# Kernel optimization log

Hardware: AMD Instinct MI355X
Metric: run time of the kernel (lower is better)

Reference implementation:

```python
import jax, jax.numpy as jnp
import numpy as np

N, D_IN, D_OUT = 100000, 256, 256
R, E, B = 8, 40000, 4
LN_EPS = 1e-5


def setup_inputs() -> dict:
    key = jax.random.key(0)
    ks = jax.random.split(key, 6)
    x = jax.random.normal(ks[0], (N, D_IN), dtype=jnp.float32)
    edge_index = jax.random.randint(ks[1], (R, 2, E), 0, N, dtype=jnp.int64)
    bases = jax.random.normal(ks[2], (B, D_IN, D_OUT), dtype=jnp.float32) * 0.01
    coefficients = jax.random.normal(ks[3], (R, B), dtype=jnp.float32) * 0.01
    bound = 1.0 / np.sqrt(D_IN)
    w_self = jax.random.uniform(ks[4], (D_IN, D_OUT), minval=-bound, maxval=bound, dtype=jnp.float32)
    b_self = jax.random.uniform(ks[5], (D_OUT,), minval=-bound, maxval=bound, dtype=jnp.float32)
    ln_gamma = jnp.ones((D_OUT,), dtype=jnp.float32)
    ln_beta = jnp.zeros((D_OUT,), dtype=jnp.float32)
    return {"x": x, "edge_index": edge_index, "bases": bases,
            "coefficients": coefficients, "w_self": w_self, "b_self": b_self,
            "ln_gamma": ln_gamma, "ln_beta": ln_beta}


def reference(x, edge_index, bases, coefficients, w_self, b_self, ln_gamma, ln_beta):
    n = x.shape[0]
    # self loop
    h = x @ w_self + b_self                                   # (N, D_OUT)
    # basis-composed per-relation weights
    W = jnp.einsum('rb,bio->rio', coefficients, bases)        # (R, D_IN, D_OUT)
    src = edge_index[:, 0]                                    # (R, E)
    dst = edge_index[:, 1]                                    # (R, E)
    msg = jnp.einsum('red,rdo->reo', x[src], W)               # (R, E, D_OUT)
    seg = jax.vmap(lambda d, m: jax.ops.segment_sum(m, d, num_segments=n))(dst, msg)
    deg = jax.vmap(lambda d: jax.ops.segment_sum(jnp.ones(d.shape, x.dtype), d, num_segments=n))(dst)
    deg = jnp.maximum(deg, 1.0)                               # clamp(min=1)
    h = h + (seg / deg[..., None]).sum(axis=0)
    # LayerNorm(SiLU(h)); dropout is identity in eval
    a = jax.nn.silu(h)
    mean = a.mean(axis=-1, keepdims=True)
    var = ((a - mean) ** 2).mean(axis=-1, keepdims=True)
    return (a - mean) * jax.lax.rsqrt(var + LN_EPS) * ln_gamma + ln_beta
```

## Files before the change

### kernel.cpp

```cpp
#include <hip/hip_runtime.h>
#include <hip/hip_bf16.h>

#define N_NODES 100000
#define D 256
#define R_REL 8
#define E_EDGES 40000
#define LN_EPS 1e-5f
#define ETOT (R_REL * E_EDGES)
#define SCAN_CH 1024
#define SCAN_NB ((N_NODES + SCAN_CH - 1) / SCAN_CH)
#define NROWT ((N_NODES + 127) / 128)
#define NWG (NROWT * 10)

typedef __attribute__((ext_vector_type(8))) short short8;
typedef __attribute__((ext_vector_type(4))) float f32x4;
typedef unsigned char uchar;

__device__ inline ushort bf16u(float f) {
    __hip_bfloat16 h = __float2bfloat16(f);
    return *reinterpret_cast<ushort*>(&h);
}
__device__ inline float bf2f(ushort u) { return __uint_as_float(((unsigned)u) << 16); }

__global__ __launch_bounds__(256) void k_prepB(const float* __restrict__ w_self,
                                               const float* __restrict__ bases,
                                               ushort* __restrict__ BT) {
    __shared__ float tile[64][65];
    int ot = blockIdx.x >> 2, dt = blockIdx.x & 3;
    int o0 = ot * 64, d0 = dt * 64;
    int m = o0 >> 8;
    const float* src = (m == 0) ? w_self : bases + (size_t)(m - 1) * D * D;
    int ol0 = o0 & 255;
    int t = threadIdx.x;
    int cl = t & 63, rw = t >> 6;
    for (int i = 0; i < 16; ++i) {
        int dl = i * 4 + rw;
        tile[dl][cl] = src[(size_t)(d0 + dl) * D + ol0 + cl];
    }
    __syncthreads();
    for (int i = 0; i < 16; ++i) {
        int ol = i * 4 + rw;
        BT[(size_t)(o0 + ol) * D + d0 + cl] = bf16u(tile[cl][ol]);
    }
}

__global__ __launch_bounds__(256) void k_prepX(const float* __restrict__ x,
                                               ushort* __restrict__ xb) {
    size_t idx = (size_t)blockIdx.x * 256 + threadIdx.x;
    const float4* xp = (const float4*)(x + idx * 8);
    float4 f0 = xp[0], f1 = xp[1];
    short8 v;
    v[0] = (short)bf16u(f0.x); v[1] = (short)bf16u(f0.y);
    v[2] = (short)bf16u(f0.z); v[3] = (short)bf16u(f0.w);
    v[4] = (short)bf16u(f1.x); v[5] = (short)bf16u(f1.y);
    v[6] = (short)bf16u(f1.z); v[7] = (short)bf16u(f1.w);
    *(short8*)(xb + idx * 8) = v;
}

__global__ void k_count(const int* __restrict__ ei, int* __restrict__ cnt) {
    int idx = blockIdx.x * blockDim.x + threadIdx.x;
    if (idx >= ETOT) return;
    int r = idx / E_EDGES, e = idx % E_EDGES;
    int dst = ei[(r * 2 + 1) * E_EDGES + e];
    atomicAdd(&cnt[dst], 1);
}

__global__ __launch_bounds__(256) void k_scanA(const int* __restrict__ cnt,
                                               int* __restrict__ start,
                                               int* __restrict__ sumsA) {
    __shared__ int sc[256];
    int t = threadIdx.x;
    int base = blockIdx.x * SCAN_CH + t * 4;
    int v0 = (base + 0 < N_NODES) ? cnt[base + 0] : 0;
    int v1 = (base + 1 < N_NODES) ? cnt[base + 1] : 0;
    int v2 = (base + 2 < N_NODES) ? cnt[base + 2] : 0;
    int v3 = (base + 3 < N_NODES) ? cnt[base + 3] : 0;
    int ts = v0 + v1 + v2 + v3;
    sc[t] = ts;
    __syncthreads();
    for (int off = 1; off < 256; off <<= 1) {
        int val = (t >= off) ? sc[t - off] : 0;
        __syncthreads();
        sc[t] += val;
        __syncthreads();
    }
    int excl = sc[t] - ts;
    if (base + 0 < N_NODES) start[base + 0] = excl;
    if (base + 1 < N_NODES) start[base + 1] = excl + v0;
    if (base + 2 < N_NODES) start[base + 2] = excl + v0 + v1;
    if (base + 3 < N_NODES) start[base + 3] = excl + v0 + v1 + v2;
    if (t == 255) sumsA[blockIdx.x] = sc[255];
}

__global__ __launch_bounds__(256) void k_scanB(const int* __restrict__ sumsA,
                                               int* __restrict__ sumsB) {
    __shared__ int sc[256];
    int t = threadIdx.x;
    int i0 = t * 4;
    int v0 = (i0 + 0 < SCAN_NB) ? sumsA[i0 + 0] : 0;
    int v1 = (i0 + 1 < SCAN_NB) ? sumsA[i0 + 1] : 0;
    int v2 = (i0 + 2 < SCAN_NB) ? sumsA[i0 + 2] : 0;
    int v3 = (i0 + 3 < SCAN_NB) ? sumsA[i0 + 3] : 0;
    int ts = v0 + v1 + v2 + v3;
    sc[t] = ts;
    __syncthreads();
    for (int off = 1; off < 256; off <<= 1) {
        int val = (t >= off) ? sc[t - off] : 0;
        __syncthreads();
        sc[t] += val;
        __syncthreads();
    }
    int excl = sc[t] - ts;
    if (i0 + 0 < SCAN_NB) sumsB[i0 + 0] = excl;
    if (i0 + 1 < SCAN_NB) sumsB[i0 + 1] = excl + v0;
    if (i0 + 2 < SCAN_NB) sumsB[i0 + 2] = excl + v0 + v1;
    if (i0 + 3 < SCAN_NB) sumsB[i0 + 3] = excl + v0 + v1 + v2;
}

__global__ __launch_bounds__(256) void k_scanC(int* __restrict__ start,
                                               const int* __restrict__ sumsB,
                                               int* __restrict__ cursor) {
    int idx = blockIdx.x * blockDim.x + threadIdx.x;
    if (idx < N_NODES) {
        int v = start[idx] + sumsB[idx / SCAN_CH];
        start[idx] = v;
        cursor[idx] = v;
    }
    if (idx == 0) start[N_NODES] = ETOT;
}

__global__ void k_scatter(const int* __restrict__ ei, int* __restrict__ cursor,
                          int* __restrict__ payload) {
    int idx = blockIdx.x * blockDim.x + threadIdx.x;
    if (idx >= ETOT) return;
    int r = idx / E_EDGES, e = idx % E_EDGES;
    int src = ei[r * 2 * E_EDGES + e];
    int dst = ei[(r * 2 + 1) * E_EDGES + e];
    int pos = atomicAdd(&cursor[dst], 1);
    payload[pos] = (r << 20) | src;
}

__global__ __launch_bounds__(256, 2) void k_gemm(const ushort* __restrict__ xb,
                                                 const ushort* __restrict__ BT,
                                                 ushort* __restrict__ hb,
                                                 uchar* __restrict__ U) {
    __shared__ ushort As[2][128 * 64];
    __shared__ ushort Bs[2][128 * 64];
    int t = threadIdx.x;

    const int q = NWG / 8, r8 = NWG % 8;
    int dd = blockIdx.x;
    int xcd = dd & 7, slot = dd >> 3;
    int wgid = (xcd < r8 ? xcd * (q + 1) : r8 * (q + 1) + (xcd - r8) * q) + slot;
    int rowtile = wgid / 10, pass = wgid % 10;
    int row0 = rowtile * 128;

    int l = t & 63, w = t >> 6;
    int wr = w >> 1, wc = w & 1;
    int lr = l & 15, lg = l >> 4;

    auto stageA = [&](int buf, int kt) {
#pragma unroll
        for (int p = 0; p < 4; ++p) {
            int o = p * 4096 + t * 16;
            int rowA = o >> 7;
            int colb = (o & 127) ^ ((rowA & 7) << 4);
            int srcrow = min(row0 + rowA, N_NODES - 1);
            const char* gp = (const char*)xb + ((size_t)srcrow * D + kt * 64) * 2 + colb;
            char* lp = (char*)&As[buf][0] + p * 4096 + (t >> 6) * 1024;
            __builtin_amdgcn_global_load_lds(
                (const __attribute__((address_space(1))) void*)gp,
                (__attribute__((address_space(3))) void*)lp, 16, 0, 0);
        }
    };
    auto stageB = [&](int buf, int kt) {
#pragma unroll
        for (int p = 0; p < 4; ++p) {
            int o = p * 4096 + t * 16;
            int rowB = o >> 7;
            int colb = (o & 127) ^ ((rowB & 7) << 4);
            const char* gp = (const char*)BT +
                ((size_t)(pass * 128 + rowB) * D + kt * 64) * 2 + colb;
            char* lp = (char*)&Bs[buf][0] + p * 4096 + (t >> 6) * 1024;
            __builtin_amdgcn_global_load_lds(
                (const __attribute__((address_space(1))) void*)gp,
                (__attribute__((address_space(3))) void*)lp, 16, 0, 0);
        }
    };

    f32x4 acc[4][4] = {};
    stageA(0, 0); stageB(0, 0);
    int buf = 0;
    for (int kt = 0; kt < 4; ++kt) {
        __syncthreads();
        if (kt < 3) { stageA(buf ^ 1, kt + 1); stageB(buf ^ 1, kt + 1); }
#pragma unroll
        for (int kk = 0; kk < 2; ++kk) {
            int kb = kk * 64 + lg * 16;
            short8 a[4], b[4];
#pragma unroll
            for (int mi = 0; mi < 4; ++mi) {
                int row = wr * 64 + mi * 16 + lr;
                a[mi] = *(const short8*)((const char*)&As[buf][0] +
                         row * 128 + (kb ^ ((row & 7) << 4)));
            }
#pragma unroll
            for (int ni = 0; ni < 4; ++ni) {
                int rb = wc * 64 + ni * 16 + lr;
                b[ni] = *(const short8*)((const char*)&Bs[buf][0] +
                         rb * 128 + (kb ^ ((rb & 7) << 4)));
            }
#pragma unroll
            for (int mi = 0; mi < 4; ++mi)
#pragma unroll
                for (int ni = 0; ni < 4; ++ni)
                    acc[mi][ni] = __builtin_amdgcn_mfma_f32_16x16x32_bf16(
                        a[mi], b[ni], acc[mi][ni], 0, 0, 0);
        }
        buf ^= 1;
    }

    if (pass < 2) {
        int colbase = pass * 128 + wc * 64 + lr;
#pragma unroll
        for (int mi = 0; mi < 4; ++mi)
#pragma unroll
            for (int j = 0; j < 4; ++j) {
                int row = row0 + wr * 64 + mi * 16 + lg * 4 + j;
                if (row < N_NODES) {
                    ushort* op = hb + (size_t)row * D + colbase;
#pragma unroll
                    for (int ni = 0; ni < 4; ++ni) op[ni * 16] = bf16u(acc[mi][ni][j]);
                }
            }
    } else {
        int pl = pass - 2;
        int plane = pl >> 1;
        int colbase = (pl & 1) * 128 + wc * 64 + lr;
#pragma unroll
        for (int mi = 0; mi < 4; ++mi)
#pragma unroll
            for (int j = 0; j < 4; ++j) {
                int row = row0 + wr * 64 + mi * 16 + lg * 4 + j;
                if (row < N_NODES) {
                    uchar* up = U + (size_t)row * 1024 + plane * 256 + colbase;
                    unsigned p01 = __builtin_amdgcn_cvt_pk_fp8_f32(
                        acc[mi][0][j] * 64.0f, acc[mi][1][j] * 64.0f, 0, 0);
                    unsigned p23 = __builtin_amdgcn_cvt_pk_fp8_f32(
                        acc[mi][2][j] * 64.0f, acc[mi][3][j] * 64.0f, 0, 0);
                    up[0]  = (uchar)(p01 & 0xFF);
                    up[16] = (uchar)((p01 >> 8) & 0xFF);
                    up[32] = (uchar)(p23 & 0xFF);
                    up[48] = (uchar)((p23 >> 8) & 0xFF);
                }
            }
    }
}

__global__ __launch_bounds__(256) void k_final(float* __restrict__ out,
                                               const ushort* __restrict__ hb,
                                               const uchar* __restrict__ U,
                                               const int* __restrict__ start,
                                               const int* __restrict__ payload,
                                               const float* __restrict__ coeff,
                                               const float* __restrict__ bias,
                                               const float* __restrict__ gamma,
                                               const float* __restrict__ beta) {
    __shared__ float cf[32];
    int t = threadIdx.x;
    if (t < 32) cf[t] = coeff[t];
    __syncthreads();
    int lane = t & 63, w = t >> 6;
    int n = blockIdx.x * 4 + w;
    int s = start[n], e = start[n + 1];

    unsigned long long cnt64 = 0;
    for (int p = s; p < e; ++p)
        cnt64 += 1ull << ((payload[p] >> 20) * 8);

    float msg[4] = {0.f, 0.f, 0.f, 0.f};
    for (int p = s; p < e; ++p) {
        int pk = payload[p];
        int r = pk >> 20, src = pk & 0xFFFFF;
        float dg = (float)((unsigned)(cnt64 >> (r * 8)) & 255u);
        float inv = __builtin_amdgcn_rcpf(dg) * 0.015625f;
        float4 wv = *(const float4*)&cf[r * 4];
        const uchar* up = U + (size_t)src * 1024 + lane * 4;
        unsigned v0 = *(const unsigned*)(up);
        unsigned v1 = *(const unsigned*)(up + 256);
        unsigned v2 = *(const unsigned*)(up + 512);
        unsigned v3 = *(const unsigned*)(up + 768);
        float w0 = wv.x * inv, w1 = wv.y * inv, w2 = wv.z * inv, w3 = wv.w * inv;
        msg[0] += w0 * __builtin_amdgcn_cvt_f32_fp8(v0, 0)
                + w1 * __builtin_amdgcn_cvt_f32_fp8(v1, 0)
                + w2 * __builtin_amdgcn_cvt_f32_fp8(v2, 0)
                + w3 * __builtin_amdgcn_cvt_f32_fp8(v3, 0);
        msg[1] += w0 * __builtin_amdgcn_cvt_f32_fp8(v0, 1)
                + w1 * __builtin_amdgcn_cvt_f32_fp8(v1, 1)
                + w2 * __builtin_amdgcn_cvt_f32_fp8(v2, 1)
                + w3 * __builtin_amdgcn_cvt_f32_fp8(v3, 1);
        msg[2] += w0 * __builtin_amdgcn_cvt_f32_fp8(v0, 2)
                + w1 * __builtin_amdgcn_cvt_f32_fp8(v1, 2)
                + w2 * __builtin_amdgcn_cvt_f32_fp8(v2, 2)
                + w3 * __builtin_amdgcn_cvt_f32_fp8(v3, 2);
        msg[3] += w0 * __builtin_amdgcn_cvt_f32_fp8(v0, 3)
                + w1 * __builtin_amdgcn_cvt_f32_fp8(v1, 3)
                + w2 * __builtin_amdgcn_cvt_f32_fp8(v2, 3)
                + w3 * __builtin_amdgcn_cvt_f32_fp8(v3, 3);
    }

    int col = lane * 4;
    size_t ro = (size_t)n * D + col;
    ushort4 hu = *(const ushort4*)&hb[ro];
    float4 bv = *(const float4*)&bias[col];
    float a[4];
    a[0] = bf2f(hu.x) + bv.x + msg[0];
    a[1] = bf2f(hu.y) + bv.y + msg[1];
    a[2] = bf2f(hu.z) + bv.z + msg[2];
    a[3] = bf2f(hu.w) + bv.w + msg[3];
    float sum = 0.f, sq = 0.f;
#pragma unroll
    for (int j = 0; j < 4; ++j) {
        a[j] = a[j] / (1.f + expf(-a[j]));
        sum += a[j]; sq += a[j] * a[j];
    }
#pragma unroll
    for (int off = 32; off >= 1; off >>= 1) {
        sum += __shfl_xor(sum, off, 64);
        sq  += __shfl_xor(sq,  off, 64);
    }
    float mean = sum * (1.0f / 256.0f);
    float var = sq * (1.0f / 256.0f) - mean * mean;
    float rs = rsqrtf(var + LN_EPS);
    float4 g4 = *(const float4*)&gamma[col];
    float4 b4 = *(const float4*)&beta[col];
    float4 o4;
    o4.x = (a[0] - mean) * rs * g4.x + b4.x;
    o4.y = (a[1] - mean) * rs * g4.y + b4.y;
    o4.z = (a[2] - mean) * rs * g4.z + b4.z;
    o4.w = (a[3] - mean) * rs * g4.w + b4.w;
    *(float4*)&out[ro] = o4;
}

extern "C" void kernel_launch(void* const* d_in, const int* in_sizes, int n_in,
                              void* d_out, int out_size, void* d_ws, size_t ws_size,
                              hipStream_t stream) {
    const float* x      = (const float*)d_in[0];
    const int*   ei     = (const int*)d_in[1];
    const float* bases  = (const float*)d_in[2];
    const float* coeff  = (const float*)d_in[3];
    const float* w_self = (const float*)d_in[4];
    const float* b_self = (const float*)d_in[5];
    const float* gamma  = (const float*)d_in[6];
    const float* beta   = (const float*)d_in[7];
    float* out = (float*)d_out;

    ushort* BT  = (ushort*)d_ws;
    ushort* xb  = BT + (size_t)1280 * D;
    ushort* hb  = xb + (size_t)N_NODES * D;
    uchar*  U   = (uchar*)(hb + (size_t)N_NODES * D);
    int* cnt    = (int*)(U + (size_t)N_NODES * 1024);
    int* start  = cnt + N_NODES;
    int* cursor = start + N_NODES + 1;
    int* sumsA  = cursor + N_NODES;
    int* sumsB  = sumsA + 128;
    int* payload = sumsB + 128;

    hipMemsetAsync(cnt, 0, (size_t)N_NODES * sizeof(int), stream);

    k_prepB<<<80, 256, 0, stream>>>(w_self, bases, BT);
    k_prepX<<<(N_NODES * D / 8 + 255) / 256, 256, 0, stream>>>(x, xb);
    k_count<<<(ETOT + 255) / 256, 256, 0, stream>>>(ei, cnt);
    k_scanA<<<SCAN_NB, 256, 0, stream>>>(cnt, start, sumsA);
    k_scanB<<<1, 256, 0, stream>>>(sumsA, sumsB);
    k_scanC<<<(N_NODES + 255) / 256, 256, 0, stream>>>(start, sumsB, cursor);
    k_scatter<<<(ETOT + 255) / 256, 256, 0, stream>>>(ei, cursor, payload);
    k_gemm<<<NWG, 256, 0, stream>>>(xb, BT, hb, U);
    k_final<<<N_NODES / 4, 256, 0, stream>>>(out, hb, U, start, payload, coeff,
                                             b_self, gamma, beta);
}
```

Before: 277.2 us.

## Transpose MFMA operands for vectorized epilogue stores; precompute per-edge inverse degree

The GEMM swaps the A/B operands of the MFMA so each lane holds four consecutive output columns. The epilogue can then write hb as ushort4 and U as packed 32-bit fp8 words instead of scattered byte and short stores. Separately, per-relation degree counts are accumulated in k_count and folded into each edge's payload as a precomputed reciprocal. This removes the extra payload pass that k_final used to rebuild per-relation degrees. In exchange, payload doubles to int2, there are more atomics into an 8xN count array, and a larger memset.

```diff
diff --git a/kernel.cpp b/kernel.cpp
--- a/kernel.cpp
+++ b/kernel.cpp
@@ -57,12 +57,14 @@
     *(short8*)(xb + idx * 8) = v;
 }
 
-__global__ void k_count(const int* __restrict__ ei, int* __restrict__ cnt) {
+__global__ void k_count(const int* __restrict__ ei, int* __restrict__ cnt,
+                        int* __restrict__ cntR) {
     int idx = blockIdx.x * blockDim.x + threadIdx.x;
     if (idx >= ETOT) return;
     int r = idx / E_EDGES, e = idx % E_EDGES;
     int dst = ei[(r * 2 + 1) * E_EDGES + e];
     atomicAdd(&cnt[dst], 1);
+    atomicAdd(&cntR[r * N_NODES + dst], 1);
 }
 
 __global__ __launch_bounds__(256) void k_scanA(const int* __restrict__ cnt,
@@ -130,14 +132,15 @@
 }
 
 __global__ void k_scatter(const int* __restrict__ ei, int* __restrict__ cursor,
-                          int* __restrict__ payload) {
+                          const int* __restrict__ cntR, int2* __restrict__ pairs) {
     int idx = blockIdx.x * blockDim.x + threadIdx.x;
     if (idx >= ETOT) return;
     int r = idx / E_EDGES, e = idx % E_EDGES;
     int src = ei[r * 2 * E_EDGES + e];
     int dst = ei[(r * 2 + 1) * E_EDGES + e];
     int pos = atomicAdd(&cursor[dst], 1);
-    payload[pos] = (r << 20) | src;
+    float invd = __builtin_amdgcn_rcpf((float)cntR[r * N_NODES + dst]) * 0.015625f;
+    pairs[pos] = make_int2((r << 20) | src, __float_as_int(invd));
 }
 
 __global__ __launch_bounds__(256, 2) void k_gemm(const ushort* __restrict__ xb,
@@ -211,47 +214,48 @@
                          rb * 128 + (kb ^ ((rb & 7) << 4)));
             }
 #pragma unroll
-            for (int mi = 0; mi < 4; ++mi)
-#pragma unroll
-                for (int ni = 0; ni < 4; ++ni)
-                    acc[mi][ni] = __builtin_amdgcn_mfma_f32_16x16x32_bf16(
-                        a[mi], b[ni], acc[mi][ni], 0, 0, 0);
+            for (int ni = 0; ni < 4; ++ni)
+#pragma unroll
+                for (int mi = 0; mi < 4; ++mi)
+                    acc[ni][mi] = __builtin_amdgcn_mfma_f32_16x16x32_bf16(
+                        b[ni], a[mi], acc[ni][mi], 0, 0, 0);
         }
         buf ^= 1;
     }
 
     if (pass < 2) {
-        int colbase = pass * 128 + wc * 64 + lr;
-#pragma unroll
-        for (int mi = 0; mi < 4; ++mi)
-#pragma unroll
-            for (int j = 0; j < 4; ++j) {
-                int row = row0 + wr * 64 + mi * 16 + lg * 4 + j;
-                if (row < N_NODES) {
-                    ushort* op = hb + (size_t)row * D + colbase;
-#pragma unroll
-                    for (int ni = 0; ni < 4; ++ni) op[ni * 16] = bf16u(acc[mi][ni][j]);
+        int colt = pass * 128 + wc * 64;
+#pragma unroll
+        for (int ni = 0; ni < 4; ++ni)
+#pragma unroll
+            for (int mi = 0; mi < 4; ++mi) {
+                int node = row0 + wr * 64 + mi * 16 + lr;
+                if (node < N_NODES) {
+                    int col = colt + ni * 16 + lg * 4;
+                    ushort4 v4;
+                    v4.x = bf16u(acc[ni][mi][0]);
+                    v4.y = bf16u(acc[ni][mi][1]);
+                    v4.z = bf16u(acc[ni][mi][2]);
+                    v4.w = bf16u(acc[ni][mi][3]);
+                    *(ushort4*)&hb[(size_t)node * D + col] = v4;
                 }
             }
     } else {
         int pl = pass - 2;
         int plane = pl >> 1;
-        int colbase = (pl & 1) * 128 + wc * 64 + lr;
-#pragma unroll
-        for (int mi = 0; mi < 4; ++mi)
-#pragma unroll
-            for (int j = 0; j < 4; ++j) {
-                int row = row0 + wr * 64 + mi * 16 + lg * 4 + j;
-                if (row < N_NODES) {
-                    uchar* up = U + (size_t)row * 1024 + plane * 256 + colbase;
-                    unsigned p01 = __builtin_amdgcn_cvt_pk_fp8_f32(
-                        acc[mi][0][j] * 64.0f, acc[mi][1][j] * 64.0f, 0, 0);
-                    unsigned p23 = __builtin_amdgcn_cvt_pk_fp8_f32(
-                        acc[mi][2][j] * 64.0f, acc[mi][3][j] * 64.0f, 0, 0);
-                    up[0]  = (uchar)(p01 & 0xFF);
-                    up[16] = (uchar)((p01 >> 8) & 0xFF);
-                    up[32] = (uchar)(p23 & 0xFF);
-                    up[48] = (uchar)((p23 >> 8) & 0xFF);
+        int colt = (pl & 1) * 128 + wc * 64;
+#pragma unroll
+        for (int ni = 0; ni < 4; ++ni)
+#pragma unroll
+            for (int mi = 0; mi < 4; ++mi) {
+                int node = row0 + wr * 64 + mi * 16 + lr;
+                if (node < N_NODES) {
+                    int col = colt + ni * 16 + lg * 4;
+                    unsigned d = __builtin_amdgcn_cvt_pk_fp8_f32(
+                        acc[ni][mi][0] * 64.0f, acc[ni][mi][1] * 64.0f, 0, false);
+                    d = __builtin_amdgcn_cvt_pk_fp8_f32(
+                        acc[ni][mi][2] * 64.0f, acc[ni][mi][3] * 64.0f, d, true);
+                    *(unsigned*)&U[(size_t)node * 1024 + plane * 256 + col] = d;
                 }
             }
     }
@@ -261,7 +265,7 @@
                                                const ushort* __restrict__ hb,
                                                const uchar* __restrict__ U,
                                                const int* __restrict__ start,
-                                               const int* __restrict__ payload,
+                                               const int2* __restrict__ pairs,
                                                const float* __restrict__ coeff,
                                                const float* __restrict__ bias,
                                                const float* __restrict__ gamma,
@@ -274,16 +278,11 @@
     int n = blockIdx.x * 4 + w;
     int s = start[n], e = start[n + 1];
 
-    unsigned long long cnt64 = 0;
-    for (int p = s; p < e; ++p)
-        cnt64 += 1ull << ((payload[p] >> 20) * 8);
-
     float msg[4] = {0.f, 0.f, 0.f, 0.f};
     for (int p = s; p < e; ++p) {
-        int pk = payload[p];
-        int r = pk >> 20, src = pk & 0xFFFFF;
-        float dg = (float)((unsigned)(cnt64 >> (r * 8)) & 255u);
-        float inv = __builtin_amdgcn_rcpf(dg) * 0.015625f;
+        int2 pw = pairs[p];
+        int r = pw.x >> 20, src = pw.x & 0xFFFFF;
+        float inv = __int_as_float(pw.y);
         float4 wv = *(const float4*)&cf[r * 4];
         const uchar* up = U + (size_t)src * 1024 + lane * 4;
         unsigned v0 = *(const unsigned*)(up);
@@ -360,22 +359,23 @@
     ushort* hb  = xb + (size_t)N_NODES * D;
     uchar*  U   = (uchar*)(hb + (size_t)N_NODES * D);
     int* cnt    = (int*)(U + (size_t)N_NODES * 1024);
-    int* start  = cnt + N_NODES;
+    int* cntR   = cnt + N_NODES;
+    int* start  = cntR + (size_t)R_REL * N_NODES;
     int* cursor = start + N_NODES + 1;
     int* sumsA  = cursor + N_NODES;
     int* sumsB  = sumsA + 128;
-    int* payload = sumsB + 128;
-
-    hipMemsetAsync(cnt, 0, (size_t)N_NODES * sizeof(int), stream);
+    int2* pairs = (int2*)(sumsB + 128);
+
+    hipMemsetAsync(cnt, 0, (size_t)(N_NODES * 9) * sizeof(int), stream);
 
     k_prepB<<<80, 256, 0, stream>>>(w_self, bases, BT);
     k_prepX<<<(N_NODES * D / 8 + 255) / 256, 256, 0, stream>>>(x, xb);
-    k_count<<<(ETOT + 255) / 256, 256, 0, stream>>>(ei, cnt);
+    k_count<<<(ETOT + 255) / 256, 256, 0, stream>>>(ei, cnt, cntR);
     k_scanA<<<SCAN_NB, 256, 0, stream>>>(cnt, start, sumsA);
     k_scanB<<<1, 256, 0, stream>>>(sumsA, sumsB);
     k_scanC<<<(N_NODES + 255) / 256, 256, 0, stream>>>(start, sumsB, cursor);
-    k_scatter<<<(ETOT + 255) / 256, 256, 0, stream>>>(ei, cursor, payload);
+    k_scatter<<<(ETOT + 255) / 256, 256, 0, stream>>>(ei, cursor, cntR, pairs);
     k_gemm<<<NWG, 256, 0, stream>>>(xb, BT, hb, U);
-    k_final<<<N_NODES / 4, 256, 0, stream>>>(out, hb, U, start, payload, coeff,
+    k_final<<<N_NODES / 4, 256, 0, stream>>>(out, hb, U, start, pairs, coeff,
                                              b_self, gamma, beta);
 }
```

Result: slower. 292.8 us (+5.6%).
